# Kernel tuning notes

Hardware: AMD Instinct MI355X
Metric: run time of the kernel (lower is better)

Reference implementation:

```python
import jax, jax.numpy as jnp
import numpy as np
from jax import lax

B, T = 8192, 4096


def setup_inputs() -> dict:
    key = jax.random.key(0)
    kx, k1, k2, k3, k4 = jax.random.split(key, 5)
    # torch.nn.RNN default init: U(-1/sqrt(hidden), 1/sqrt(hidden)) = U(-1, 1) for hidden=1
    u = lambda k, shp: jax.random.uniform(k, shp, jnp.float32, -1.0, 1.0)
    return {
        "x": jax.random.normal(kx, (B, T, 1), jnp.float32),
        "w_ih": u(k1, (1, 1)),
        "w_hh": u(k2, (1, 1)),
        "b_ih": u(k3, (1,)),
        "b_hh": u(k4, (1,)),
    }


def reference(x, w_ih, w_hh, b_ih, b_hh):
    # Vanilla tanh RNN: h_t = tanh(x_t @ W_ih^T + b_ih + h_{t-1} @ W_hh^T + b_hh)
    # hidden=input=1, so all matmuls are scalar multiplies. Output is h at last step.
    a = w_ih[0, 0]
    b = w_hh[0, 0]
    c = b_ih[0] + b_hh[0]
    xT = jnp.swapaxes(x, 0, 1)  # [T, B, 1]

    def step(h, x_t):
        h_new = jnp.tanh(x_t * a + h * b + c)
        return h_new, None

    h0 = jnp.zeros((x.shape[0], 1), x.dtype)
    hT, _ = lax.scan(step, h0, xT)
    return hT  # [B, 1], equals rnn_output[:, -1]
```

## Files before the change

### kernel.cpp

```cpp
#include <hip/hip_runtime.h>


constexpr int T_LEN = 4096;
constexpr int NTHR  = 256;
constexpr int CH    = T_LEN / NTHR;
constexpr int NF4   = CH / 4;

typedef float fx4 __attribute__((ext_vector_type(4)));

__device__ __forceinline__ int swz(int s) { return s ^ ((s >> 2) & 7); }

#define STEP_PG(qv)                                                     \
    do {                                                                \
        float r_ = __builtin_amdgcn_rcpf(E + 1.0f);                     \
        P *= (fourb * r_) * (1.0f - r_);                                \
        E = __builtin_amdgcn_exp2f(fmaf(r_, nB4, (qv)));                \
    } while (0)

__global__ __launch_bounds__(NTHR)
void rnn_row_kernel(const float* __restrict__ x,
                    const float* __restrict__ w_ih,
                    const float* __restrict__ w_hh,
                    const float* __restrict__ b_ih,
                    const float* __restrict__ b_hh,
                    float* __restrict__ out) {
    __shared__ fx4 sm[T_LEN / 4];
    __shared__ float wP[4], wG[4];

    const int tid  = threadIdx.x;
    const int lane = tid & 63;
    const int wv   = tid >> 6;
    const int row  = blockIdx.x;

    const float a  = w_ih[0];
    const float bb = w_hh[0];
    const float cc = b_ih[0] + b_hh[0];

    const float L2E2  = 2.88539008177792681472f;
    const float A2    = a * L2E2;
    const float C2    = (bb + cc) * L2E2;
    const float nB4   = -(bb * L2E2 * 2.0f);
    const float fourb = 4.0f * bb;

    const fx4* xp = (const fx4*)(x + (size_t)row * T_LEN);
#pragma unroll
    for (int i = 0; i < 4; ++i) {
        int s = i * NTHR + tid;
        sm[swz(s)] = xp[s];
    }
    __syncthreads();

    fx4 buf[NF4];
#pragma unroll
    for (int q = 0; q < NF4; ++q) buf[q] = sm[swz(tid * NF4 + q)];

    float E, P = 1.0f;
    {
        fx4 v = buf[0];
        float q0 = fmaf(v.x, A2, C2);
        float q1 = fmaf(v.y, A2, C2);
        float q2 = fmaf(v.z, A2, C2);
        float q3 = fmaf(v.w, A2, C2);
        E = __builtin_amdgcn_exp2f(fmaf(0.5f, nB4, q0));
        STEP_PG(q1); STEP_PG(q2); STEP_PG(q3);
    }
#pragma unroll
    for (int i = 1; i < NF4; ++i) {
        fx4 v = buf[i];
        float q0 = fmaf(v.x, A2, C2);
        float q1 = fmaf(v.y, A2, C2);
        float q2 = fmaf(v.z, A2, C2);
        float q3 = fmaf(v.w, A2, C2);
        STEP_PG(q0); STEP_PG(q1); STEP_PG(q2); STEP_PG(q3);
    }
    float r = __builtin_amdgcn_rcpf(E + 1.0f);
    float G = fmaf(-2.0f, r, 1.0f);
    P *= (fourb * r) * (1.0f - r);

#pragma unroll
    for (int d = 1; d < 64; d <<= 1) {
        float Pl = __shfl_up(P, d, 64);
        float Gl = __shfl_up(G, d, 64);
        if (lane >= d) {
            G = fmaf(P, Gl, G);
            P *= Pl;
        }
    }
    if (lane == 63) { wP[wv] = P; wG[wv] = G; }
    __syncthreads();

    if (tid == 0) {
        float h = wG[0];
        h = fmaf(wP[1], h, wG[1]);
        h = fmaf(wP[2], h, wG[2]);
        h = fmaf(wP[3], h, wG[3]);
        out[row] = h;
    }
}

extern "C" void kernel_launch(void* const* d_in, const int* in_sizes, int n_in,
                              void* d_out, int out_size, void* d_ws, size_t ws_size,
                              hipStream_t stream) {
    const float* x    = (const float*)d_in[0];
    const float* w_ih = (const float*)d_in[1];
    const float* w_hh = (const float*)d_in[2];
    const float* b_ih = (const float*)d_in[3];
    const float* b_hh = (const float*)d_in[4];
    float* out = (float*)d_out;

    const int B = out_size;
    dim3 grid(B), block(NTHR);
    rnn_row_kernel<<<grid, block, 0, stream>>>(x, w_ih, w_hh, b_ih, b_hh, out);
}
```

Measured before the change: 191.9 us.

## Process four rows per block with per-wave quarter-row chunks and nontemporal loads

Each block now handles four rows; each wave owns a quarter of every row, loading it into its own shared-memory slice and scanning it, looping over the four rows. The block-wide barrier between load and compute is removed, loads become nontemporal, and launch bounds request higher occupancy. This aims to cut per-block launch and synchronisation overhead, but serialises row processing within a wave and may expose load latency per row.

```diff
diff --git a/kernel.cpp b/kernel.cpp
--- a/kernel.cpp
+++ b/kernel.cpp
@@ -3,12 +3,12 @@
 
 constexpr int T_LEN = 4096;
 constexpr int NTHR  = 256;
-constexpr int CH    = T_LEN / NTHR;
-constexpr int NF4   = CH / 4;
+constexpr int RPB   = 4;
+constexpr int QF4   = 256;
 
 typedef float fx4 __attribute__((ext_vector_type(4)));
 
-__device__ __forceinline__ int swz(int s) { return s ^ ((s >> 2) & 7); }
+__device__ __forceinline__ int swzl(int s) { return s ^ ((s >> 2) & 7); }
 
 #define STEP_PG(qv)                                                     \
     do {                                                                \
@@ -17,20 +17,20 @@
         E = __builtin_amdgcn_exp2f(fmaf(r_, nB4, (qv)));                \
     } while (0)
 
-__global__ __launch_bounds__(NTHR)
-void rnn_row_kernel(const float* __restrict__ x,
-                    const float* __restrict__ w_ih,
-                    const float* __restrict__ w_hh,
-                    const float* __restrict__ b_ih,
-                    const float* __restrict__ b_hh,
-                    float* __restrict__ out) {
-    __shared__ fx4 sm[T_LEN / 4];
-    __shared__ float wP[4], wG[4];
+__global__ __launch_bounds__(NTHR, 8)
+void rnn_rows_kernel(const float* __restrict__ x,
+                     const float* __restrict__ w_ih,
+                     const float* __restrict__ w_hh,
+                     const float* __restrict__ b_ih,
+                     const float* __restrict__ b_hh,
+                     float* __restrict__ out) {
+    __shared__ fx4 sm[4][QF4];
+    __shared__ float pgP[RPB][4], pgG[RPB][4];
 
     const int tid  = threadIdx.x;
     const int lane = tid & 63;
     const int wv   = tid >> 6;
-    const int row  = blockIdx.x;
+    const int row0 = blockIdx.x * RPB;
 
     const float a  = w_ih[0];
     const float bb = w_hh[0];
@@ -42,59 +42,64 @@
     const float nB4   = -(bb * L2E2 * 2.0f);
     const float fourb = 4.0f * bb;
 
-    const fx4* xp = (const fx4*)(x + (size_t)row * T_LEN);
+    const fx4* xq = (const fx4*)x + (size_t)row0 * (T_LEN / 4) + wv * QF4;
+
+    for (int r = 0; r < RPB; ++r) {
+        const fx4* xr = xq + (size_t)r * (T_LEN / 4);
+
 #pragma unroll
-    for (int i = 0; i < 4; ++i) {
-        int s = i * NTHR + tid;
-        sm[swz(s)] = xp[s];
+        for (int i = 0; i < 4; ++i) {
+            int s = i * 64 + lane;
+            sm[wv][swzl(s)] = __builtin_nontemporal_load(&xr[s]);
+        }
+
+        fx4 buf[4];
+#pragma unroll
+        for (int q = 0; q < 4; ++q) buf[q] = sm[wv][swzl(4 * lane + q)];
+
+        float E, P = 1.0f;
+        {
+            fx4 v = buf[0];
+            float q0 = fmaf(v.x, A2, C2);
+            float q1 = fmaf(v.y, A2, C2);
+            float q2 = fmaf(v.z, A2, C2);
+            float q3 = fmaf(v.w, A2, C2);
+            E = __builtin_amdgcn_exp2f(fmaf(0.5f, nB4, q0));
+            STEP_PG(q1); STEP_PG(q2); STEP_PG(q3);
+        }
+#pragma unroll
+        for (int i = 1; i < 4; ++i) {
+            fx4 v = buf[i];
+            float q0 = fmaf(v.x, A2, C2);
+            float q1 = fmaf(v.y, A2, C2);
+            float q2 = fmaf(v.z, A2, C2);
+            float q3 = fmaf(v.w, A2, C2);
+            STEP_PG(q0); STEP_PG(q1); STEP_PG(q2); STEP_PG(q3);
+        }
+        float rr = __builtin_amdgcn_rcpf(E + 1.0f);
+        float G  = fmaf(-2.0f, rr, 1.0f);
+        P *= (fourb * rr) * (1.0f - rr);
+
+#pragma unroll
+        for (int d = 1; d < 64; d <<= 1) {
+            float Pl = __shfl_up(P, d, 64);
+            float Gl = __shfl_up(G, d, 64);
+            if (lane >= d) {
+                G = fmaf(P, Gl, G);
+                P *= Pl;
+            }
+        }
+        if (lane == 63) { pgP[r][wv] = P; pgG[r][wv] = G; }
     }
+
     __syncthreads();
 
-    fx4 buf[NF4];
-#pragma unroll
-    for (int q = 0; q < NF4; ++q) buf[q] = sm[swz(tid * NF4 + q)];
-
-    float E, P = 1.0f;
-    {
-        fx4 v = buf[0];
-        float q0 = fmaf(v.x, A2, C2);
-        float q1 = fmaf(v.y, A2, C2);
-        float q2 = fmaf(v.z, A2, C2);
-        float q3 = fmaf(v.w, A2, C2);
-        E = __builtin_amdgcn_exp2f(fmaf(0.5f, nB4, q0));
-        STEP_PG(q1); STEP_PG(q2); STEP_PG(q3);
-    }
-#pragma unroll
-    for (int i = 1; i < NF4; ++i) {
-        fx4 v = buf[i];
-        float q0 = fmaf(v.x, A2, C2);
-        float q1 = fmaf(v.y, A2, C2);
-        float q2 = fmaf(v.z, A2, C2);
-        float q3 = fmaf(v.w, A2, C2);
-        STEP_PG(q0); STEP_PG(q1); STEP_PG(q2); STEP_PG(q3);
-    }
-    float r = __builtin_amdgcn_rcpf(E + 1.0f);
-    float G = fmaf(-2.0f, r, 1.0f);
-    P *= (fourb * r) * (1.0f - r);
-
-#pragma unroll
-    for (int d = 1; d < 64; d <<= 1) {
-        float Pl = __shfl_up(P, d, 64);
-        float Gl = __shfl_up(G, d, 64);
-        if (lane >= d) {
-            G = fmaf(P, Gl, G);
-            P *= Pl;
-        }
-    }
-    if (lane == 63) { wP[wv] = P; wG[wv] = G; }
-    __syncthreads();
-
-    if (tid == 0) {
-        float h = wG[0];
-        h = fmaf(wP[1], h, wG[1]);
-        h = fmaf(wP[2], h, wG[2]);
-        h = fmaf(wP[3], h, wG[3]);
-        out[row] = h;
+    if (tid < RPB) {
+        float h = pgG[tid][0];
+        h = fmaf(pgP[tid][1], h, pgG[tid][1]);
+        h = fmaf(pgP[tid][2], h, pgG[tid][2]);
+        h = fmaf(pgP[tid][3], h, pgG[tid][3]);
+        out[row0 + tid] = h;
     }
 }
 
@@ -109,6 +114,6 @@
     float* out = (float*)d_out;
 
     const int B = out_size;
-    dim3 grid(B), block(NTHR);
-    rnn_row_kernel<<<grid, block, 0, stream>>>(x, w_ih, w_hh, b_ih, b_hh, out);
+    dim3 grid(B / RPB), block(NTHR);
+    rnn_rows_kernel<<<grid, block, 0, stream>>>(x, w_ih, w_hh, b_ih, b_hh, out);
 }
```

Result: faster. 184.3 us (-4.0%).
